# Optimization experiments

Measured on AMD Instinct MI355X. Metric: run time of the kernel, lower is better.

## Reference

```python
import jax, jax.numpy as jnp
import numpy as np

B, CIN, COUT, K, H, W = 16, 128, 256, 3, 56, 56
STRIDE = 1
PAD = K // 2


def setup_inputs() -> dict:
    key = jax.random.key(0)
    ks = jax.random.split(key, 12)
    x = jax.random.normal(ks[0], (B, CIN, H, W), dtype=jnp.float32)
    base_kernel = jax.random.normal(ks[1], (COUT, CIN, K, K), dtype=jnp.float32)
    bias = jnp.zeros((COUT,), dtype=jnp.float32)
    s = 1.0 / np.sqrt(CIN)
    fc_spatial_w = jax.random.uniform(ks[2], (K * K, CIN), minval=-s, maxval=s)
    fc_spatial_b = jax.random.uniform(ks[3], (K * K,), minval=-s, maxval=s)
    fc_in_w = jax.random.uniform(ks[4], (CIN, CIN), minval=-s, maxval=s)
    fc_in_b = jax.random.uniform(ks[5], (CIN,), minval=-s, maxval=s)
    fc_out_w = jax.random.uniform(ks[6], (COUT, CIN), minval=-s, maxval=s)
    fc_out_b = jax.random.uniform(ks[7], (COUT,), minval=-s, maxval=s)
    fc_kernel_w = jax.random.uniform(ks[8], (COUT * CIN * K * K, CIN), minval=-s, maxval=s)
    fc_kernel_b = jax.random.uniform(ks[9], (COUT * CIN * K * K,), minval=-s, maxval=s)
    return {
        "x": x, "base_kernel": base_kernel, "bias": bias,
        "fc_spatial_w": fc_spatial_w, "fc_spatial_b": fc_spatial_b,
        "fc_in_w": fc_in_w, "fc_in_b": fc_in_b,
        "fc_out_w": fc_out_w, "fc_out_b": fc_out_b,
        "fc_kernel_w": fc_kernel_w, "fc_kernel_b": fc_kernel_b,
    }


def _odconv(x, base_kernel, bias, fc_spatial_w, fc_spatial_b, fc_in_w, fc_in_b,
            fc_out_w, fc_out_b, fc_kernel_w, fc_kernel_b):
    b = x.shape[0]
    # global average pool -> context [B, Cin]
    context = jnp.mean(x, axis=(2, 3))
    sig = jax.nn.sigmoid
    attn_spatial = sig(context @ fc_spatial_w.T + fc_spatial_b).reshape(b, 1, 1, K, K)
    attn_in = sig(context @ fc_in_w.T + fc_in_b).reshape(b, 1, CIN, 1, 1)
    attn_out = sig(context @ fc_out_w.T + fc_out_b).reshape(b, COUT, 1, 1, 1)
    attn_kernel = sig(context @ fc_kernel_w.T + fc_kernel_b).reshape(b, COUT, CIN, K, K)
    # 5-way broadcast multiply -> per-sample dynamic kernel [B, Cout, Cin, K, K]
    dyn = base_kernel[None] * attn_out * attn_in * attn_spatial * attn_kernel

    def conv_one(xi, wi):
        # xi: [Cin, H, W], wi: [Cout, Cin, K, K]
        out = jax.lax.conv_general_dilated(
            xi[None], wi,
            window_strides=(STRIDE, STRIDE),
            padding=[(PAD, PAD), (PAD, PAD)],
            dimension_numbers=("NCHW", "OIHW", "NCHW"),
        )
        return out[0]

    out = jax.vmap(conv_one)(x, dyn)  # [B, Cout, H', W']
    return out + bias[None, :, None, None]


def reference(x, base_kernel, bias, fc_spatial_w, fc_spatial_b, fc_in_w, fc_in_b,
              fc_out_w, fc_out_b, fc_kernel_w, fc_kernel_b):
    return _odconv(x, base_kernel, bias, fc_spatial_w, fc_spatial_b, fc_in_w, fc_in_b,
                   fc_out_w, fc_out_b, fc_kernel_w, fc_kernel_b)
```

## Files before the change

### kernel.cpp

```cpp
#include <hip/hip_runtime.h>
#include <hip/hip_bf16.h>
#include <math.h>

#define BATCH 16
#define CIN   128
#define COUT  256
#define HH    56
#define WW    56
#define HW    3136
#define NTAP  9
#define NE    (COUT*CIN*NTAP)

typedef short short8 __attribute__((ext_vector_type(8)));
typedef float floatx4 __attribute__((ext_vector_type(4)));

#define WSB_CTX   0
#define WSB_ASP   8192
#define WSB_AIN   9472
#define WSB_AOUT  17664
#define WSB_ZP    34048
#define WSB_XT    38144
#define WSB_DYN   (WSB_XT + BATCH*HW*CIN*2)

static __device__ inline unsigned short f2b(float f) {
    union { float f; unsigned u; } v; v.f = f;
    unsigned r = v.u + 0x7FFF + ((v.u >> 16) & 1);
    return (unsigned short)(r >> 16);
}
static __device__ inline short8 pack8(float4 a, float4 b) {
    short8 r;
    r[0] = (short)f2b(a.x); r[1] = (short)f2b(a.y); r[2] = (short)f2b(a.z); r[3] = (short)f2b(a.w);
    r[4] = (short)f2b(b.x); r[5] = (short)f2b(b.y); r[6] = (short)f2b(b.z); r[7] = (short)f2b(b.w);
    return r;
}

typedef const __attribute__((address_space(1))) void* gas_ptr;
typedef __attribute__((address_space(3))) void* las_ptr;
static __device__ __forceinline__ void gl_lds16(const void* g, void* l) {
    __builtin_amdgcn_global_load_lds((gas_ptr)g, (las_ptr)l, 16, 0, 0);
}

__global__ void k_context(const float* __restrict__ x, float* __restrict__ ctx,
                          float* __restrict__ zp) {
    int bc = blockIdx.x;
    if (bc == 0 && threadIdx.x < 64) {
        uint4 z = {0u, 0u, 0u, 0u};
        ((uint4*)zp)[threadIdx.x] = z;
    }
    const float4* p = (const float4*)(x + (size_t)bc * HW);
    float s = 0.f;
    for (int i = threadIdx.x; i < HW / 4; i += 256) { float4 v = p[i]; s += v.x + v.y + v.z + v.w; }
    for (int off = 32; off; off >>= 1) s += __shfl_down(s, off, 64);
    __shared__ float red[4];
    if ((threadIdx.x & 63) == 0) red[threadIdx.x >> 6] = s;
    __syncthreads();
    if (threadIdx.x == 0) ctx[bc] = (red[0] + red[1] + red[2] + red[3]) * (1.f / (float)HW);
}

__global__ void k_attn(const float* __restrict__ ctx,
                       const float* __restrict__ wsp, const float* __restrict__ bsp,
                       const float* __restrict__ win, const float* __restrict__ bin,
                       const float* __restrict__ wout, const float* __restrict__ bout,
                       float* __restrict__ asp, float* __restrict__ ain, float* __restrict__ aout) {
    int R = blockIdx.x * 4 + (threadIdx.x >> 6);
    int lane = threadIdx.x & 63;
    int b = R / 393, r = R % 393;
    const float* w; float bias; float* o;
    if (r < 9)        { w = wsp  + r * CIN;         bias = bsp[r];         o = asp  + b * 16  + r; }
    else if (r < 137) { w = win  + (r - 9) * CIN;   bias = bin[r - 9];     o = ain  + b * CIN + (r - 9); }
    else              { w = wout + (r - 137) * CIN; bias = bout[r - 137];  o = aout + b * COUT + (r - 137); }
    float2 wv = ((const float2*)w)[lane];
    float2 cv = ((const float2*)(ctx + b * CIN))[lane];
    float d = wv.x * cv.x + wv.y * cv.y;
    for (int off = 32; off; off >>= 1) d += __shfl_down(d, off, 64);
    if (lane == 0) *o = 1.f / (1.f + __expf(-(d + bias)));
}

#define XT_V2_BLOCKS (BATCH * 4 * 13)
__global__ __launch_bounds__(256) void k_xt(const float* __restrict__ x,
                                            unsigned short* __restrict__ xt) {
    __shared__ unsigned short s[32 * 264];
    int bid = blockIdx.x;
    int b = bid / 52, rem = bid % 52;
    int chg = rem / 13, ck = rem % 13;
    int px0 = ck * 256;
    int npx = HW - px0; if (npx > 256) npx = 256;
    int tid = threadIdx.x;
    const float* xb = x + ((size_t)(b * CIN + chg * 32)) * HW + px0;
#pragma unroll
    for (int pass = 0; pass < 8; ++pass) {
        int i = pass * 256 + tid;
        int c = i >> 6, p4 = i & 63;
        int px = p4 * 4;
        if (px < npx) {
            float4 v = *(const float4*)(xb + (size_t)c * HW + px);
            unsigned short h[4] = {f2b(v.x), f2b(v.y), f2b(v.z), f2b(v.w)};
            *(uint2*)(&s[c * 264 + px]) = *(const uint2*)h;
        }
    }
    __syncthreads();
    int px = tid;
    if (px < npx) {
        unsigned short h[32];
#pragma unroll
        for (int c = 0; c < 32; ++c) h[c] = s[c * 264 + px];
        uint4* dst = (uint4*)(xt + ((size_t)b * HW + px0 + px) * CIN + chg * 32);
        const uint4* q = (const uint4*)h;
        dst[0] = q[0]; dst[1] = q[1]; dst[2] = q[2]; dst[3] = q[3];
    }
}

#define BUILD_BLOCKS 1152
__global__ __launch_bounds__(256, 4) void k_build(
    const float* __restrict__ ctx, const float* __restrict__ wk,
    const float* __restrict__ bk, const float* __restrict__ base,
    const float* __restrict__ asp, const float* __restrict__ ain,
    const float* __restrict__ aout, unsigned short* __restrict__ dyn) {
    __shared__ unsigned short s_res[9 * 530 + 16];
    int bid = blockIdx.x;
    int wid = threadIdx.x >> 6, l = threadIdx.x & 63;
    int lq = l & 15, quad = l >> 4;
    int e0      = bid * 256;
    int siteMin = e0 / 9;

    short8 afr[4];
    const float* arow = ctx + lq * CIN;
#pragma unroll
    for (int kc = 0; kc < 4; ++kc) {
        float4 v0 = *(const float4*)(arow + kc * 32 + quad * 8);
        float4 v1 = *(const float4*)(arow + kc * 32 + quad * 8 + 4);
        afr[kc] = pack8(v0, v1);
    }

    int ebase = e0 + wid * 64;
#pragma unroll
    for (int jp = 0; jp < 2; ++jp) {
        short8 bfr[2][4];
        float bke[2], bse[2];
        floatx4 acc[2];
#pragma unroll
        for (int u = 0; u < 2; ++u) {
            int j = jp * 2 + u;
            unsigned e = ebase + j * 16 + lq;
            const float* wrow = wk + (size_t)e * CIN;
#pragma unroll
            for (int kc = 0; kc < 4; ++kc) {
                float4 v0 = *(const float4*)(wrow + kc * 32 + quad * 8);
                float4 v1 = *(const float4*)(wrow + kc * 32 + quad * 8 + 4);
                bfr[u][kc] = pack8(v0, v1);
            }
            bke[u] = bk[e]; bse[u] = base[e];
            acc[u] = (floatx4){0.f, 0.f, 0.f, 0.f};
        }
#pragma unroll
        for (int u = 0; u < 2; ++u)
#pragma unroll
            for (int kc = 0; kc < 4; ++kc)
                acc[u] = __builtin_amdgcn_mfma_f32_16x16x32_bf16(afr[kc], bfr[u][kc], acc[u], 0, 0, 0);
#pragma unroll
        for (int u = 0; u < 2; ++u) {
            int j = jp * 2 + u;
            unsigned e = ebase + j * 16 + lq;
            unsigned site = e / 9u, tap = e - site * 9u;
            unsigned oc = site >> 7, ic = site & 127;
            unsigned ds = site - siteMin;
#pragma unroll
            for (int r = 0; r < 4; ++r) {
                int bb = quad * 4 + r;
                float sg = 1.f / (1.f + __expf(-(acc[u][r] + bke[u])));
                float v = bse[u] * sg * aout[bb * COUT + oc] * ain[bb * CIN + ic] * asp[bb * 16 + tap];
                s_res[tap * 530 + bb * 32 + ds] = f2b(v);
            }
        }
    }
    __syncthreads();
    int hw_id = threadIdx.x >> 5;
    int hl    = threadIdx.x & 31;
#pragma unroll
    for (int it = 0; it < 18; ++it) {
        int pair = it * 8 + hw_id;
        int t = pair >> 4, b = pair & 15;
        int sLo = (e0 - t + 8) / 9;
        int sHi = (e0 + 255 - t) / 9;
        int cnt = sHi - sLo + 1;
        if (hl < cnt) {
            unsigned short v = s_res[t * 530 + b * 32 + (sLo - siteMin) + hl];
            dyn[(size_t)b * NE + t * 32768 + sLo + hl] = v;
        }
    }
}

__global__ __launch_bounds__(256, 2) void k_conv(
    const unsigned short* __restrict__ xt, const unsigned short* __restrict__ dyn,
    const float* __restrict__ bias, float* __restrict__ out,
    const unsigned short* __restrict__ zp) {
    __shared__ char s_x[640 * 64];
    __shared__ char s_a[576 * 64];
    int id  = blockIdx.x;
    int low = id & 7;
    int q   = id >> 3;
    int r   = q % 7;
    int phi = q / 7;
    int p   = phi * 8 + low;
    int oc0 = (p >> 4) * 64;
    int b   = p & 15;
    int r0  = r * 8;

    int tid = threadIdx.x;
    int wn = tid >> 6, l = tid & 63, lq = l & 15, quad = l >> 4;
    const unsigned short* xtb  = xt  + (size_t)b * HW * CIN;
    const unsigned short* dynb = dyn + (size_t)b * NE;

    int colx = wn * 16 + (l >> 2);
    int gxs  = colx - 1;
    bool gxok = (unsigned)gxs < (unsigned)WW;
    const unsigned short* zsrc = zp + l * 8;

    int pixaddr[7];
#pragma unroll
    for (int nf = 0; nf < 7; ++nf) {
        int n = nf * 16 + lq;
        int tr = wn * 2 + n / 56, col = n % 56;
        pixaddr[nf] = (tr * 64 + col) * 64 + quad * 16;
    }

    floatx4 acc[4][7];
#pragma unroll
    for (int i = 0; i < 4; ++i)
#pragma unroll
        for (int j = 0; j < 7; ++j) acc[i][j] = (floatx4){0.f, 0.f, 0.f, 0.f};

    for (int kc = 0; kc < 4; ++kc) {
        __syncthreads();
#pragma unroll
        for (int ry = 0; ry < 10; ++ry) {
            int gy = r0 + ry - 1;
            const unsigned short* src =
                (gxok && (unsigned)gy < (unsigned)HH)
                    ? xtb + (size_t)(gy * WW + gxs) * CIN + kc * 32 + (l & 3) * 8
                    : zsrc;
            gl_lds16(src, s_x + ry * 4096 + wn * 1024);
        }
#pragma unroll
        for (int i = 0; i < 9; ++i) {
            int u = i * 256 + tid;
            int icq2 = u & 3, oc = (u >> 2) & 63, tap = u >> 8;
            gl_lds16(dynb + (size_t)(tap * COUT + oc0 + oc) * CIN + kc * 32 + icq2 * 8,
                     s_a + i * 4096 + wn * 1024);
        }
        __syncthreads();
        __builtin_amdgcn_s_setprio(1);
#pragma unroll
        for (int tap = 0; tap < 9; ++tap) {
            short8 af[4];
#pragma unroll
            for (int mf = 0; mf < 4; ++mf)
                af[mf] = *(const short8*)(s_a + (tap * 64 + mf * 16 + lq) * 64 + quad * 16);
            int toff = (tap / 3) * 4096 + (tap % 3) * 64;
#pragma unroll
            for (int nf = 0; nf < 7; ++nf) {
                short8 bf = *(const short8*)(s_x + pixaddr[nf] + toff);
#pragma unroll
                for (int mf = 0; mf < 4; ++mf)
                    acc[mf][nf] = __builtin_amdgcn_mfma_f32_16x16x32_bf16(af[mf], bf, acc[mf][nf], 0, 0, 0);
            }
        }
        __builtin_amdgcn_s_setprio(0);
    }

#pragma unroll
    for (int mf = 0; mf < 4; ++mf) {
#pragma unroll
        for (int rr = 0; rr < 4; ++rr) {
            int oc = oc0 + mf * 16 + quad * 4 + rr;
            float bs = bias[oc];
            float* ob = out + (size_t)(b * COUT + oc) * HW + (r0 + wn * 2) * 56 + lq;
#pragma unroll
            for (int nf = 0; nf < 7; ++nf)
                ob[nf * 16] = acc[mf][nf][rr] + bs;
        }
    }
}

extern "C" void kernel_launch(void* const* d_in, const int* in_sizes, int n_in,
                              void* d_out, int out_size, void* d_ws, size_t ws_size,
                              hipStream_t stream) {
    const float* x    = (const float*)d_in[0];
    const float* base = (const float*)d_in[1];
    const float* bias = (const float*)d_in[2];
    const float* wsp  = (const float*)d_in[3];
    const float* bsp  = (const float*)d_in[4];
    const float* win  = (const float*)d_in[5];
    const float* bin  = (const float*)d_in[6];
    const float* wout = (const float*)d_in[7];
    const float* bout = (const float*)d_in[8];
    const float* wk   = (const float*)d_in[9];
    const float* bk   = (const float*)d_in[10];
    float* out = (float*)d_out;
    char* ws = (char*)d_ws;

    float* ctx  = (float*)(ws + WSB_CTX);
    float* asp  = (float*)(ws + WSB_ASP);
    float* ain  = (float*)(ws + WSB_AIN);
    float* aout = (float*)(ws + WSB_AOUT);
    float* zp   = (float*)(ws + WSB_ZP);
    unsigned short* xt  = (unsigned short*)(ws + WSB_XT);
    unsigned short* dyn = (unsigned short*)(ws + WSB_DYN);

    k_context<<<BATCH * CIN, 256, 0, stream>>>(x, ctx, zp);
    k_attn<<<(BATCH * 393) / 4, 256, 0, stream>>>(ctx, wsp, bsp, win, bin, wout, bout, asp, ain, aout);
    k_xt<<<XT_V2_BLOCKS, 256, 0, stream>>>(x, xt);
    k_build<<<BUILD_BLOCKS, 256, 0, stream>>>(ctx, wk, bk, base, asp, ain, aout, dyn);
    k_conv<<<448, 256, 0, stream>>>(xt, dyn, bias, out, (const unsigned short*)zp);
}
```

Before: 313.5 us.

## Stage fc_kernel weights through swizzled LDS with direct global-to-LDS loads

Reworks k_build to load the 256x128 fp32 fc_kernel_w tile for each block in four 32-column chunks. Each chunk goes straight from global memory into a swizzled shared buffer via gl_lds16, instead of every lane doing strided float4 global loads per row. Each wave then reads its B fragments from LDS with an XOR swizzle to avoid bank conflicts. The goal is fully coalesced reads of this ~150MB weight stream, which dominates the kernel. The cost is 32KB of extra LDS per block, a lower occupancy hint (launch_bounds 4 to 3), and extra barriers per chunk.

```diff
diff --git a/kernel.cpp b/kernel.cpp
--- a/kernel.cpp
+++ b/kernel.cpp
@@ -111,17 +111,27 @@
 }
 
 #define BUILD_BLOCKS 1152
-__global__ __launch_bounds__(256, 4) void k_build(
+__global__ __launch_bounds__(256, 3) void k_build(
     const float* __restrict__ ctx, const float* __restrict__ wk,
     const float* __restrict__ bk, const float* __restrict__ base,
     const float* __restrict__ asp, const float* __restrict__ ain,
     const float* __restrict__ aout, unsigned short* __restrict__ dyn) {
+    __shared__ float s_wk[256 * 32];
     __shared__ unsigned short s_res[9 * 530 + 16];
     int bid = blockIdx.x;
-    int wid = threadIdx.x >> 6, l = threadIdx.x & 63;
+    int tid = threadIdx.x;
+    int wid = tid >> 6, l = tid & 63;
     int lq = l & 15, quad = l >> 4;
     int e0      = bid * 256;
     int siteMin = e0 / 9;
+    int ebase   = e0 + wid * 64;
+
+    float bke[4], bse[4];
+#pragma unroll
+    for (int j = 0; j < 4; ++j) {
+        unsigned e = ebase + j * 16 + lq;
+        bke[j] = bk[e]; bse[j] = base[e];
+    }
 
     short8 afr[4];
     const float* arow = ctx + lq * CIN;
@@ -132,45 +142,46 @@
         afr[kc] = pack8(v0, v1);
     }
 
-    int ebase = e0 + wid * 64;
-#pragma unroll
-    for (int jp = 0; jp < 2; ++jp) {
-        short8 bfr[2][4];
-        float bke[2], bse[2];
-        floatx4 acc[2];
-#pragma unroll
-        for (int u = 0; u < 2; ++u) {
-            int j = jp * 2 + u;
-            unsigned e = ebase + j * 16 + lq;
-            const float* wrow = wk + (size_t)e * CIN;
-#pragma unroll
-            for (int kc = 0; kc < 4; ++kc) {
-                float4 v0 = *(const float4*)(wrow + kc * 32 + quad * 8);
-                float4 v1 = *(const float4*)(wrow + kc * 32 + quad * 8 + 4);
-                bfr[u][kc] = pack8(v0, v1);
-            }
-            bke[u] = bk[e]; bse[u] = base[e];
-            acc[u] = (floatx4){0.f, 0.f, 0.f, 0.f};
-        }
-#pragma unroll
-        for (int u = 0; u < 2; ++u)
-#pragma unroll
-            for (int kc = 0; kc < 4; ++kc)
-                acc[u] = __builtin_amdgcn_mfma_f32_16x16x32_bf16(afr[kc], bfr[u][kc], acc[u], 0, 0, 0);
-#pragma unroll
-        for (int u = 0; u < 2; ++u) {
-            int j = jp * 2 + u;
-            unsigned e = ebase + j * 16 + lq;
-            unsigned site = e / 9u, tap = e - site * 9u;
-            unsigned oc = site >> 7, ic = site & 127;
-            unsigned ds = site - siteMin;
-#pragma unroll
-            for (int r = 0; r < 4; ++r) {
-                int bb = quad * 4 + r;
-                float sg = 1.f / (1.f + __expf(-(acc[u][r] + bke[u])));
-                float v = bse[u] * sg * aout[bb * COUT + oc] * ain[bb * CIN + ic] * asp[bb * 16 + tap];
-                s_res[tap * 530 + bb * 32 + ds] = f2b(v);
-            }
+    int pp = l & 7, h = pp >> 1, lo = pp & 1;
+
+    floatx4 acc[4];
+#pragma unroll
+    for (int j = 0; j < 4; ++j) acc[j] = (floatx4){0.f, 0.f, 0.f, 0.f};
+
+    for (int kc = 0; kc < 4; ++kc) {
+        __syncthreads();
+#pragma unroll
+        for (int i = 0; i < 8; ++i) {
+            int row = i * 32 + wid * 8 + (l >> 3);
+            int sp  = ((h ^ (row & 3)) << 1) | lo;
+            const float* src = wk + ((size_t)(e0 + row) << 7) + kc * 32 + sp * 4;
+            gl_lds16(src, (char*)s_wk + i * 4096 + wid * 1024);
+        }
+        __syncthreads();
+#pragma unroll
+        for (int j = 0; j < 4; ++j) {
+            int r  = wid * 64 + j * 16 + lq;
+            int hs = quad ^ (r & 3);
+            const char* pb = (const char*)s_wk + r * 128 + hs * 32;
+            float4 v0 = *(const float4*)pb;
+            float4 v1 = *(const float4*)(pb + 16);
+            short8 bfr = pack8(v0, v1);
+            acc[j] = __builtin_amdgcn_mfma_f32_16x16x32_bf16(afr[kc], bfr, acc[j], 0, 0, 0);
+        }
+    }
+
+#pragma unroll
+    for (int j = 0; j < 4; ++j) {
+        unsigned e = ebase + j * 16 + lq;
+        unsigned site = e / 9u, tap = e - site * 9u;
+        unsigned oc = site >> 7, ic = site & 127;
+        unsigned ds = site - siteMin;
+#pragma unroll
+        for (int r = 0; r < 4; ++r) {
+            int bb = quad * 4 + r;
+            float sg = 1.f / (1.f + __expf(-(acc[j][r] + bke[j])));
+            float v = bse[j] * sg * aout[bb * COUT + oc] * ain[bb * CIN + ic] * asp[bb * 16 + tap];
+            s_res[tap * 530 + bb * 32 + ds] = f2b(v);
         }
     }
     __syncthreads();
```

After: 318.0 us. No clear change (+1.4%).

## Swizzle LDS tiles in conv kernel and stage attention factors in shared memory

Applied to the files above, without the earlier changes.

The conv kernel now XOR-swizzles the 16-byte channel pieces of the input and dynamic-kernel tiles. The swizzle is applied when the global-to-LDS copies run and undone in the MFMA fragment reads, which is meant to remove LDS bank conflicts. The build kernel also preloads the per-block slices of aout, ain and the spatial attention into shared memory, replacing scattered global loads in the inner epilogue. In exchange it keeps more precomputed per-tap address registers (7x3), which may raise register pressure, and adds an extra barrier in the build kernel.

```diff
diff --git a/kernel.cpp b/kernel.cpp
--- a/kernel.cpp
+++ b/kernel.cpp
@@ -116,12 +116,28 @@
     const float* __restrict__ bk, const float* __restrict__ base,
     const float* __restrict__ asp, const float* __restrict__ ain,
     const float* __restrict__ aout, unsigned short* __restrict__ dyn) {
+    __shared__ float s_ao[16 * 31];
+    __shared__ float s_ai[16 * 31];
+    __shared__ float s_as[16 * 12];
     __shared__ unsigned short s_res[9 * 530 + 16];
     int bid = blockIdx.x;
-    int wid = threadIdx.x >> 6, l = threadIdx.x & 63;
+    int tid = threadIdx.x;
+    int wid = tid >> 6, l = tid & 63;
     int lq = l & 15, quad = l >> 4;
     int e0      = bid * 256;
     int siteMin = e0 / 9;
+    int ebase   = e0 + wid * 64;
+
+    for (int t = tid; t < 496; t += 256) {
+        int b = t / 31, ds = t - b * 31;
+        int site = siteMin + ds;
+        s_ao[t] = aout[b * COUT + (site >> 7)];
+        s_ai[t] = ain[b * CIN + (site & 127)];
+    }
+    if (tid < 144) {
+        int b = tid / 9, tp = tid - b * 9;
+        s_as[b * 12 + tp] = asp[b * 16 + tp];
+    }
 
     short8 afr[4];
     const float* arow = ctx + lq * CIN;
@@ -131,8 +147,8 @@
         float4 v1 = *(const float4*)(arow + kc * 32 + quad * 8 + 4);
         afr[kc] = pack8(v0, v1);
     }
-
-    int ebase = e0 + wid * 64;
+    __syncthreads();
+
 #pragma unroll
     for (int jp = 0; jp < 2; ++jp) {
         short8 bfr[2][4];
@@ -162,13 +178,13 @@
             int j = jp * 2 + u;
             unsigned e = ebase + j * 16 + lq;
             unsigned site = e / 9u, tap = e - site * 9u;
-            unsigned oc = site >> 7, ic = site & 127;
             unsigned ds = site - siteMin;
 #pragma unroll
             for (int r = 0; r < 4; ++r) {
                 int bb = quad * 4 + r;
                 float sg = 1.f / (1.f + __expf(-(acc[u][r] + bke[u])));
-                float v = bse[u] * sg * aout[bb * COUT + oc] * ain[bb * CIN + ic] * asp[bb * 16 + tap];
+                float v = bse[u] * sg * s_ao[bb * 31 + ds] * s_ai[bb * 31 + ds]
+                          * s_as[bb * 12 + tap];
                 s_res[tap * 530 + bb * 32 + ds] = f2b(v);
             }
         }
@@ -215,14 +231,21 @@
     int gxs  = colx - 1;
     bool gxok = (unsigned)gxs < (unsigned)WW;
     const unsigned short* zsrc = zp + l * 8;
-
-    int pixaddr[7];
+    int pieceq = (l & 3) ^ ((colx + (colx >> 2)) & 3);
+
+    int pixaddr3[7][3];
 #pragma unroll
     for (int nf = 0; nf < 7; ++nf) {
         int n = nf * 16 + lq;
         int tr = wn * 2 + n / 56, col = n % 56;
-        pixaddr[nf] = (tr * 64 + col) * 64 + quad * 16;
-    }
+        int rb = (tr * 64 + col) * 64;
+#pragma unroll
+        for (int m = 0; m < 3; ++m) {
+            int cc = col + m;
+            pixaddr3[nf][m] = rb + m * 64 + ((quad ^ ((cc + (cc >> 2)) & 3)) << 4);
+        }
+    }
+    int sA = quad ^ ((lq + (lq >> 2)) & 3);
 
     floatx4 acc[4][7];
 #pragma unroll
@@ -237,15 +260,16 @@
             int gy = r0 + ry - 1;
             const unsigned short* src =
                 (gxok && (unsigned)gy < (unsigned)HH)
-                    ? xtb + (size_t)(gy * WW + gxs) * CIN + kc * 32 + (l & 3) * 8
+                    ? xtb + (size_t)(gy * WW + gxs) * CIN + kc * 32 + pieceq * 8
                     : zsrc;
             gl_lds16(src, s_x + ry * 4096 + wn * 1024);
         }
 #pragma unroll
         for (int i = 0; i < 9; ++i) {
             int u = i * 256 + tid;
-            int icq2 = u & 3, oc = (u >> 2) & 63, tap = u >> 8;
-            gl_lds16(dynb + (size_t)(tap * COUT + oc0 + oc) * CIN + kc * 32 + icq2 * 8,
+            int sp = u & 3, oc = (u >> 2) & 63, tap = u >> 8;
+            int qa = sp ^ ((oc + (oc >> 2)) & 3);
+            gl_lds16(dynb + (size_t)(tap * COUT + oc0 + oc) * CIN + kc * 32 + qa * 8,
                      s_a + i * 4096 + wn * 1024);
         }
         __syncthreads();
@@ -255,11 +279,12 @@
             short8 af[4];
 #pragma unroll
             for (int mf = 0; mf < 4; ++mf)
-                af[mf] = *(const short8*)(s_a + (tap * 64 + mf * 16 + lq) * 64 + quad * 16);
-            int toff = (tap / 3) * 4096 + (tap % 3) * 64;
+                af[mf] = *(const short8*)(s_a + (tap * 64 + mf * 16 + lq) * 64 + (sA << 4));
+            int toffr = (tap / 3) * 4096;
+            int mtap = tap % 3;
 #pragma unroll
             for (int nf = 0; nf < 7; ++nf) {
-                short8 bf = *(const short8*)(s_x + pixaddr[nf] + toff);
+                short8 bf = *(const short8*)(s_x + pixaddr3[nf][mtap] + toffr);
 #pragma unroll
                 for (int mf = 0; mf < 4; ++mf)
                     acc[mf][nf] = __builtin_amdgcn_mfma_f32_16x16x32_bf16(af[mf], bf, acc[mf][nf], 0, 0, 0);
```

New measurement: 334.7 us. 6.8% more time.
